# Kernel tuning notes

Measured on AMD Instinct MI355X. Metric: run time of the kernel, lower is better.

## Reference

```python
import jax, jax.numpy as jnp
import numpy as np

N_HEADS = 16
KV_HEADS = 4
HEAD_DIM = 128
D_MODEL = N_HEADS * HEAD_DIM  # 2048
KV_DIM = KV_HEADS * HEAD_DIM  # 512
MAX_POS = 4096
ROPE_THETA = 10000.0
EPS = 1e-5


def _rope_cache(seq_len):
    # QEffMolmoRotaryEmbedding: inv_freq over head_dim, emb = cat(freqs, freqs)
    inv_freq = 1.0 / (ROPE_THETA ** (jnp.arange(0, HEAD_DIM, 2, dtype=jnp.float32) / HEAD_DIM))
    t = jnp.arange(seq_len, dtype=jnp.float32)
    freqs = jnp.outer(t, inv_freq)                      # [S, D/2]
    emb = jnp.concatenate([freqs, freqs], axis=-1)      # [S, D]
    return jnp.cos(emb), jnp.sin(emb)


def _rotate_half(x):
    # x: [B, H, T, D] -> cat(-x2, x1) with halves along last dim
    x1, x2 = jnp.split(x, 2, axis=-1)
    return jnp.concatenate([-x2, x1], axis=-1)


def _rms_norm(x, w):
    var = jnp.mean(jnp.square(x), axis=-1, keepdims=True)
    return (x * jax.lax.rsqrt(var + EPS)) * w


def setup_inputs() -> dict:
    key = jax.random.key(0)
    ks = jax.random.split(key, 8)
    B, T = 1, 2048
    q = jax.random.normal(ks[0], (B, T, D_MODEL), dtype=jnp.float32)
    k = jax.random.normal(ks[1], (B, T, KV_DIM), dtype=jnp.float32)
    v = jax.random.normal(ks[2], (B, T, KV_DIM), dtype=jnp.float32)
    # causal mask: True means masked (torch.where(mask, -10000, scores))
    attention_mask = jnp.triu(jnp.ones((T, T), dtype=bool), k=1)[None, None]  # [1,1,T,T]
    position_ids = jnp.arange(T, dtype=jnp.int32)[None, :]                    # [B,T]
    q_norm_w = jax.random.normal(ks[3], (D_MODEL,), dtype=jnp.float32) * 0.02 + 1.0
    k_norm_w = jax.random.normal(ks[4], (KV_DIM,), dtype=jnp.float32) * 0.02 + 1.0
    w_out = jax.random.normal(ks[5], (D_MODEL, D_MODEL), dtype=jnp.float32) * (D_MODEL ** -0.5)
    return {"q": q, "k": k, "v": v, "attention_mask": attention_mask,
            "position_ids": position_ids, "q_norm_w": q_norm_w,
            "k_norm_w": k_norm_w, "w_out": w_out}


def reference(q, k, v, attention_mask, position_ids, q_norm_w, k_norm_w, w_out):
    B, T, C = q.shape
    # QK-norm on flat projections
    q = _rms_norm(q, q_norm_w)
    k = _rms_norm(k, k_norm_w)
    # split heads: [B, H, T, D]
    q = q.reshape(B, T, N_HEADS, HEAD_DIM).transpose(0, 2, 1, 3)
    k = k.reshape(B, T, KV_HEADS, HEAD_DIM).transpose(0, 2, 1, 3)
    v = v.reshape(B, T, KV_HEADS, HEAD_DIM).transpose(0, 2, 1, 3)
    # RoPE (rotate_half variant)
    cos_c, sin_c = _rope_cache(MAX_POS)
    cos = cos_c[position_ids][:, None]  # [B,1,T,D]
    sin = sin_c[position_ids][:, None]
    q = q * cos + _rotate_half(q) * sin
    k = k * cos + _rotate_half(k) * sin
    # GQA expand
    rep = N_HEADS // KV_HEADS
    k = jnp.repeat(k, rep, axis=1)
    v = jnp.repeat(v, rep, axis=1)
    scale = 1.0 / np.sqrt(HEAD_DIM)
    scores = jnp.einsum('bhqd,bhkd->bhqk', q, k) * scale  # [B,H,T,T]
    scores = jnp.where(attention_mask, jnp.float32(-10000.0), scores)
    attn = jax.nn.softmax(scores.astype(jnp.float32), axis=-1).astype(q.dtype)
    out = jnp.einsum('bhqk,bhkd->bhqd', attn, v)          # [B,H,T,D]
    out = out.transpose(0, 2, 1, 3).reshape(B, T, C)
    return out @ w_out.T
```

## Files before the change

### kernel.cpp

```cpp
#include <hip/hip_runtime.h>
#include <hip/hip_bf16.h>
#include <math.h>

#define T_SEQ 2048
#define NH 16
#define KVH 4
#define HD 128
#define DM 2048
#define KVD 512

typedef short bf16x8 __attribute__((ext_vector_type(8)));
typedef float f32x4 __attribute__((ext_vector_type(4)));
typedef float f32x16 __attribute__((ext_vector_type(16)));
typedef unsigned int uint2v __attribute__((ext_vector_type(2)));

static __device__ __forceinline__ unsigned short f2bf(float f) {
    unsigned int x = __float_as_uint(f);
    x += 0x7fff + ((x >> 16) & 1);
    return (unsigned short)(x >> 16);
}
static __device__ __forceinline__ float bf2f(unsigned short u) {
    return __uint_as_float(((unsigned int)u) << 16);
}

static __device__ __forceinline__ unsigned int cvtpk(float lo, float hi) {
    unsigned int r;
    asm("v_cvt_pk_bf16_f32 %0, %1, %2" : "=v"(r) : "v"(lo), "v"(hi));
    return r;
}

static __device__ __forceinline__ f32x4 mfma16(bf16x8 a, bf16x8 b, f32x4 c) {
    return __builtin_amdgcn_mfma_f32_16x16x32_bf16(a, b, c, 0, 0, 0);
}
static __device__ __forceinline__ f32x16 mfma32(bf16x8 a, bf16x8 b, f32x16 c) {
    return __builtin_amdgcn_mfma_f32_32x32x16_bf16(a, b, c, 0, 0, 0);
}

static __device__ __forceinline__ void gl_lds16(const unsigned short* g, unsigned short* l) {
    __builtin_amdgcn_global_load_lds(
        (const __attribute__((address_space(1))) unsigned int*)g,
        (__attribute__((address_space(3))) unsigned int*)l,
        16, 0, 0);
}


__global__ __launch_bounds__(256) void qk_prep(
    const float* __restrict__ q, const float* __restrict__ k,
    const float* __restrict__ qw, const float* __restrict__ kw,
    const int* __restrict__ pos_ids,
    unsigned short* __restrict__ Qb, unsigned short* __restrict__ Ks) {
    __shared__ float qr[DM];
    __shared__ float kr[KVD];
    __shared__ float cosL[64], sinL[64];
    __shared__ float redq[4], redk[4];
    int t = blockIdx.x, tid = threadIdx.x;

    float qs = 0.f, ks = 0.f;
    {
        const float* qp = q + (size_t)t * DM + tid * 8;
        float4 v0 = *(const float4*)(qp);
        float4 v1 = *(const float4*)(qp + 4);
        float* dst = qr + tid * 8;
        dst[0] = v0.x; dst[1] = v0.y; dst[2] = v0.z; dst[3] = v0.w;
        dst[4] = v1.x; dst[5] = v1.y; dst[6] = v1.z; dst[7] = v1.w;
        qs = v0.x * v0.x + v0.y * v0.y + v0.z * v0.z + v0.w * v0.w +
             v1.x * v1.x + v1.y * v1.y + v1.z * v1.z + v1.w * v1.w;
        float2 kv = *(const float2*)(k + (size_t)t * KVD + tid * 2);
        kr[tid * 2] = kv.x; kr[tid * 2 + 1] = kv.y;
        ks = kv.x * kv.x + kv.y * kv.y;
    }
    if (tid < 64) {
        float pos = (float)pos_ids[t];
        float inv = powf(10000.0f, -(float)tid * (1.0f / 64.0f));
        float a = pos * inv;
        cosL[tid] = cosf(a);
        sinL[tid] = sinf(a);
    }
    for (int off = 32; off; off >>= 1) {
        qs += __shfl_down(qs, off);
        ks += __shfl_down(ks, off);
    }
    if ((tid & 63) == 0) { redq[tid >> 6] = qs; redk[tid >> 6] = ks; }
    __syncthreads();
    float qinv = rsqrtf((redq[0] + redq[1] + redq[2] + redq[3]) * (1.0f / DM) + 1e-5f);
    float kinv = rsqrtf((redk[0] + redk[1] + redk[2] + redk[3]) * (1.0f / KVD) + 1e-5f);

    {
        int base = tid * 8;
        int h = base >> 7;
        int d = base & 127;
        bool lo = d < 64;
        int i0 = d & 63;
        int pb = lo ? base + 64 : base - 64;
        #pragma unroll
        for (int j = 0; j < 8; ++j) {
            float xv = qr[base + j] * qinv * qw[base + j];
            float pv = qr[pb + j] * qinv * qw[pb + j];
            float c = cosL[i0 + j];
            float s = sinL[i0 + j];
            float o = lo ? (xv * c - pv * s) : (xv * c + pv * s);
            Qb[((size_t)h * T_SEQ + t) * HD + d + j] = f2bf(o);
        }
    }
    {
        int base = tid * 2;
        int kh = base >> 7;
        int d = base & 127;
        bool lo = d < 64;
        int i0 = d & 63;
        int pb = lo ? base + 64 : base - 64;
        int kt = t >> 5, lq = t & 31;
        #pragma unroll
        for (int j = 0; j < 2; ++j) {
            float xv = kr[base + j] * kinv * kw[base + j];
            float pv = kr[pb + j] * kinv * kw[pb + j];
            float c = cosL[i0 + j];
            float s = sinL[i0 + j];
            float o = lo ? (xv * c - pv * s) : (xv * c + pv * s);
            int dj = d + j;
            int sl = dj >> 4, hi2 = (dj >> 3) & 1, jj = dj & 7;
            size_t oi = ((((size_t)(kh * 64 + kt) * 8 + sl) * 2 + hi2) * 32 + lq) * 8 + jj;
            Ks[oi] = f2bf(o);
        }
    }
}

__global__ __launch_bounds__(256) void vw_prep(const float* __restrict__ v,
                                               unsigned short* __restrict__ Vs,
                                               const float* __restrict__ w,
                                               unsigned short* __restrict__ Wb) {
    int bid = blockIdx.x;
    int tid = threadIdx.x;
    if (bid < 4096) {
        size_t idx = ((size_t)bid * 256 + tid) * 4;
        float4 f = *(const float4*)(w + idx);
        ushort4 o;
        o.x = f2bf(f.x); o.y = f2bf(f.y); o.z = f2bf(f.z); o.w = f2bf(f.w);
        *(ushort4*)(Wb + idx) = o;
        return;
    }
    __shared__ unsigned short tile[64][80];
    int vb = bid - 4096;
    int tb = vb & 31;
    int cb = vb >> 5;
    #pragma unroll 4
    for (int rep = 0; rep < 16; ++rep) {
        int e = rep * 256 + tid;
        int r = e >> 6;
        int c = e & 63;
        tile[c][r] = f2bf(v[(size_t)(tb * 64 + r) * KVD + cb * 64 + c]);
    }
    __syncthreads();
    #pragma unroll
    for (int rep = 0; rep < 2; ++rep) {
        int e = rep * 256 + tid;
        int cc = e >> 3, tg = e & 7;
        int cg = cb * 64 + cc;
        int kh = cg >> 7, crow = cg & 127, db = crow >> 5, lq = crow & 31;
        int t0g = tb * 64 + tg * 8;
        int kt = t0g >> 5, tr = t0g & 31, half = tr >> 4, hi2 = (tr >> 3) & 1;
        size_t o = (((((size_t)(kh * 64 + kt) * 2 + half) * 4 + db) * 2 + hi2) * 32 + lq) * 8;
        *(bf16x8*)(Vs + o) = *(const bf16x8*)(&tile[cc][tg * 8]);
    }
}

#define BEXP 20.0f
#define SCALE2 (0.08838834764831845f * 1.4426950408889634f)

#define STAGE1(B, S, KT)                                                           \
    do {                                                                           \
        const unsigned short* kg_ = Kt_g + (size_t)(KT) * 4096;                    \
        const unsigned short* vg_ = Vt_g + (size_t)(KT) * 4096;                    \
        gl_lds16(kg_ + w * 512 + l * 8,        &kv[B][S][w * 512]);                \
        gl_lds16(kg_ + 2048 + w * 512 + l * 8, &kv[B][S][2048 + w * 512]);         \
        gl_lds16(vg_ + w * 512 + l * 8,        &kv[B][S][4096 + w * 512]);         \
        gl_lds16(vg_ + 2048 + w * 512 + l * 8, &kv[B][S][6144 + w * 512]);         \
    } while (0)

#define TILE_COMPUTE(BUF, SLOT, KT)                                                \
    do {                                                                           \
        const unsigned short* kl = &kv[BUF][SLOT][0] + l * 8;                      \
        const unsigned short* vl = &kv[BUF][SLOT][4096] + l * 8;                   \
        f32x16 sa, sb;                                                             \
        _Pragma("unroll") for (int r = 0; r < 16; ++r) { sa[r] = 0.f; sb[r] = 0.f; } \
        _Pragma("unroll") for (int x = 0; x < 8; x += 2) {                         \
            bf16x8 k0 = *(const bf16x8*)(kl + x * 512);                            \
            bf16x8 k1 = *(const bf16x8*)(kl + (x + 1) * 512);                      \
            sa = mfma32(k0, qf[x], sa);                                            \
            sb = mfma32(k1, qf[x + 1], sb);                                        \
        }                                                                          \
        float p_[16];                                                              \
        if ((KT) == nkt - 1) {                                                     \
            int lim = qglob - (KT) * 32;                                           \
            _Pragma("unroll") for (int r = 0; r < 16; ++r) {                       \
                float e_ = __builtin_amdgcn_exp2f((sa[r] + sb[r]) * SCALE2 - BEXP); \
                int off_ = (r & 3) + 8 * (r >> 2) + 4 * hi;                        \
                p_[r] = (off_ <= lim) ? e_ : 0.f;                                  \
                sden4[r & 3] += p_[r];                                             \
            }                                                                      \
        } else {                                                                   \
            _Pragma("unroll") for (int r = 0; r < 16; ++r) {                       \
                p_[r] = __builtin_amdgcn_exp2f((sa[r] + sb[r]) * SCALE2 - BEXP);   \
                sden4[r & 3] += p_[r];                                             \
            }                                                                      \
        }                                                                          \
        _Pragma("unroll") for (int half = 0; half < 2; ++half) {                   \
            unsigned int a0 = cvtpk(p_[half * 8 + 0], p_[half * 8 + 1]);           \
            unsigned int a1 = cvtpk(p_[half * 8 + 2], p_[half * 8 + 3]);           \
            unsigned int b0 = cvtpk(p_[half * 8 + 4], p_[half * 8 + 5]);           \
            unsigned int b1 = cvtpk(p_[half * 8 + 6], p_[half * 8 + 7]);           \
            uint2v w0 = __builtin_amdgcn_permlane32_swap(a0, b0, false, false);    \
            uint2v w1 = __builtin_amdgcn_permlane32_swap(a1, b1, false, false);    \
            union { unsigned int u[4]; bf16x8 v; } pc;                             \
            pc.u[0] = w0[0]; pc.u[1] = w1[0]; pc.u[2] = w0[1]; pc.u[3] = w1[1];    \
            bf16x8 pf = pc.v;                                                      \
            _Pragma("unroll") for (int db = 0; db < 4; ++db) {                     \
                bf16x8 vf = *(const bf16x8*)(vl + (half * 4 + db) * 512);          \
                oacc[db] = mfma32(vf, pf, oacc[db]);                               \
            }                                                                      \
        }                                                                          \
    } while (0)

__global__ __launch_bounds__(256) void attn_fwd18(
    const unsigned short* __restrict__ Qb, const unsigned short* __restrict__ Ks,
    const unsigned short* __restrict__ Vs,
    unsigned short* __restrict__ Opart, float* __restrict__ Lpart,
    unsigned short* __restrict__ Xo, int CHUNK) {
    int qrow = 63 - (int)blockIdx.x;
    int kh = blockIdx.y;
    int seg = blockIdx.z;
    int tid = threadIdx.x;
    int w = tid >> 6, l = tid & 63;
    int h = kh * 4 + w;
    int lq = l & 31, hi = l >> 5;
    int qglob = qrow * 32 + lq;

    int nkt = qrow + 1;
    int t0 = seg * CHUNK;
    int t1 = min(t0 + CHUNK, nkt);
    if (t0 >= t1) return;
    size_t idx = (size_t)(h * 64 + qrow) * 4 + seg;

    const unsigned short* Qh = Qb + (size_t)h * T_SEQ * HD;
    const unsigned short* Kt_g = Ks + (size_t)kh * 64 * 4096;
    const unsigned short* Vt_g = Vs + (size_t)kh * 64 * 4096;

    __shared__ unsigned short kv[2][2][8192];

    bf16x8 qf[8];
    #pragma unroll
    for (int sl = 0; sl < 8; ++sl)
        qf[sl] = *(const bf16x8*)(Qh + (size_t)qglob * HD + sl * 16 + hi * 8);

    f32x16 oacc[4];
    #pragma unroll
    for (int db = 0; db < 4; ++db)
        #pragma unroll
        for (int r = 0; r < 16; ++r) oacc[db][r] = 0.f;
    f32x4 sden4 = (f32x4){0.f, 0.f, 0.f, 0.f};

    int pairsEnd = t0 + ((t1 - t0) & ~1);
    int kt = t0;
    int cur = 0;
    if (kt < pairsEnd) { STAGE1(0, 0, kt); STAGE1(0, 1, kt + 1); }
    if (kt + 2 < pairsEnd) { STAGE1(1, 0, kt + 2); STAGE1(1, 1, kt + 3); }
    for (; kt < pairsEnd; kt += 2) {
        bool more = (kt + 2 < pairsEnd);
        if (more) asm volatile("s_waitcnt vmcnt(8)" ::: "memory");
        else      asm volatile("s_waitcnt vmcnt(0)" ::: "memory");
        __builtin_amdgcn_s_barrier();
        TILE_COMPUTE(cur, 0, kt);
        TILE_COMPUTE(cur, 1, kt + 1);
        asm volatile("s_waitcnt lgkmcnt(0)" ::: "memory");
        __builtin_amdgcn_s_barrier();
        if (kt + 4 < pairsEnd) { STAGE1(cur, 0, kt + 4); STAGE1(cur, 1, kt + 5); }
        cur ^= 1;
    }
    if (kt < t1) {
        STAGE1(cur, 0, kt);
        asm volatile("s_waitcnt vmcnt(0)" ::: "memory");
        __builtin_amdgcn_s_barrier();
        TILE_COMPUTE(cur, 0, kt);
    }

    float sden = (sden4[0] + sden4[1]) + (sden4[2] + sden4[3]);
    float sden_tot = sden + __shfl_xor(sden, 32);

    if (t0 == 0 && t1 == nkt) {
        float invs = 1.0f / sden_tot;
        #pragma unroll
        for (int db = 0; db < 4; ++db) {
            #pragma unroll
            for (int r = 0; r < 16; ++r) {
                int d = db * 32 + (r & 3) + 8 * (r >> 2) + 4 * hi;
                Xo[(size_t)qglob * DM + h * HD + d] = f2bf(oacc[db][r] * invs);
            }
        }
        return;
    }
    if (hi == 0) Lpart[idx * 32 + lq] = sden_tot;
    unsigned short* op = Opart + (idx << 12);
    #pragma unroll
    for (int db = 0; db < 4; ++db) {
        #pragma unroll
        for (int r = 0; r < 16; ++r) {
            int d = db * 32 + (r & 3) + 8 * (r >> 2) + 4 * hi;
            op[d * 32 + lq] = f2bf(oacc[db][r]);
        }
    }
}

__global__ __launch_bounds__(256) void attn_combine(
    const unsigned short* __restrict__ Opart, const float* __restrict__ Lpart,
    unsigned short* __restrict__ Xo, int CHUNK) {
    int qrow = CHUNK + blockIdx.x;
    int h = blockIdx.y;
    int tid = threadIdx.x;
    int nkt = qrow + 1;
    int used = (nkt + CHUNK - 1) / CHUNK;
    int base = (h * 64 + qrow) * 4;
    __shared__ float invden[32];
    if (tid < 32) {
        int q = tid;
        float den = 0.f;
        for (int s = 0; s < used; ++s) den += Lpart[(base + s) * 32 + q];
        invden[q] = 1.0f / den;
    }
    __syncthreads();
    int d = tid >> 1, q0 = (tid & 1) * 16;
    float acc[16];
    #pragma unroll
    for (int j = 0; j < 16; ++j) acc[j] = 0.f;
    for (int s = 0; s < used; ++s) {
        const unsigned short* op = Opart + ((size_t)(base + s) << 12) + d * 32 + q0;
        bf16x8 o0 = *(const bf16x8*)(op);
        bf16x8 o1 = *(const bf16x8*)(op + 8);
        #pragma unroll
        for (int j = 0; j < 8; ++j) {
            acc[j]     += bf2f((unsigned short)o0[j]);
            acc[8 + j] += bf2f((unsigned short)o1[j]);
        }
    }
    __shared__ unsigned short xo[32][136];
    #pragma unroll
    for (int j = 0; j < 16; ++j)
        xo[q0 + j][d] = f2bf(acc[j] * invden[q0 + j]);
    __syncthreads();
    int q = tid >> 3, dc = (tid & 7) * 16;
    bf16x8 v0 = *(const bf16x8*)(&xo[q][dc]);
    bf16x8 v1 = *(const bf16x8*)(&xo[q][dc + 8]);
    size_t ro = (size_t)(qrow * 32 + q) * DM + h * HD + dc;
    *(bf16x8*)(Xo + ro) = v0;
    *(bf16x8*)(Xo + ro + 8) = v1;
}

__global__ __launch_bounds__(256) void outproj2(
    const unsigned short* __restrict__ X, const unsigned short* __restrict__ Wb,
    float* __restrict__ out) {
    __shared__ unsigned short As[128][72];
    __shared__ unsigned short Bs[64][72];
    int tid = threadIdx.x;
    int w = tid >> 6, l = tid & 63;
    int lr = l & 15, lg = l >> 4;
    int wm = w >> 1, wn = w & 1;
    int id = blockIdx.x;
    int wg = (id & 7) * 64 + (id >> 3);
    int s = wg >> 5, wi = wg & 31;
    int mb = (s & 3) * 4 + (wi & 3);
    int nb = (s >> 2) * 8 + (wi >> 2);
    int m0 = mb * 128, n0 = nb * 64;

    int ar_row[4], ar_col[4], br_row[2], br_col[2];
    #pragma unroll
    for (int qd = 0; qd < 4; ++qd) {
        int c = tid + qd * 256;
        ar_row[qd] = c >> 3; ar_col[qd] = (c & 7) * 8;
    }
    #pragma unroll
    for (int qd = 0; qd < 2; ++qd) {
        int c = tid + qd * 256;
        br_row[qd] = c >> 3; br_col[qd] = (c & 7) * 8;
    }

    f32x4 acc[4][2];
    #pragma unroll
    for (int i = 0; i < 4; ++i)
        #pragma unroll
        for (int j = 0; j < 2; ++j) acc[i][j] = (f32x4){0.f, 0.f, 0.f, 0.f};

    bf16x8 ar[4], br[2];
    #pragma unroll
    for (int qd = 0; qd < 4; ++qd)
        ar[qd] = *(const bf16x8*)(X + (size_t)(m0 + ar_row[qd]) * DM + ar_col[qd]);
    #pragma unroll
    for (int qd = 0; qd < 2; ++qd)
        br[qd] = *(const bf16x8*)(Wb + (size_t)(n0 + br_row[qd]) * DM + br_col[qd]);
    #pragma unroll
    for (int qd = 0; qd < 4; ++qd)
        *(bf16x8*)(&As[ar_row[qd]][ar_col[qd]]) = ar[qd];
    #pragma unroll
    for (int qd = 0; qd < 2; ++qd)
        *(bf16x8*)(&Bs[br_row[qd]][br_col[qd]]) = br[qd];
    __syncthreads();

    for (int t = 0; t < DM / 64; ++t) {
        if (t + 1 < DM / 64) {
            int k0 = (t + 1) * 64;
            #pragma unroll
            for (int qd = 0; qd < 4; ++qd)
                ar[qd] = *(const bf16x8*)(X + (size_t)(m0 + ar_row[qd]) * DM + k0 + ar_col[qd]);
            #pragma unroll
            for (int qd = 0; qd < 2; ++qd)
                br[qd] = *(const bf16x8*)(Wb + (size_t)(n0 + br_row[qd]) * DM + k0 + br_col[qd]);
        }
        #pragma unroll
        for (int ks = 0; ks < 2; ++ks) {
            bf16x8 af[4], bfr[2];
            #pragma unroll
            for (int i = 0; i < 4; ++i)
                af[i] = *(const bf16x8*)(&As[wm * 64 + i * 16 + lr][ks * 32 + lg * 8]);
            #pragma unroll
            for (int j = 0; j < 2; ++j)
                bfr[j] = *(const bf16x8*)(&Bs[wn * 32 + j * 16 + lr][ks * 32 + lg * 8]);
            #pragma unroll
            for (int i = 0; i < 4; ++i)
                #pragma unroll
                for (int j = 0; j < 2; ++j)
                    acc[i][j] = mfma16(af[i], bfr[j], acc[i][j]);
        }
        if (t + 1 < DM / 64) {
            __syncthreads();
            #pragma unroll
            for (int qd = 0; qd < 4; ++qd)
                *(bf16x8*)(&As[ar_row[qd]][ar_col[qd]]) = ar[qd];
            #pragma unroll
            for (int qd = 0; qd < 2; ++qd)
                *(bf16x8*)(&Bs[br_row[qd]][br_col[qd]]) = br[qd];
            __syncthreads();
        }
    }
    #pragma unroll
    for (int i = 0; i < 4; ++i) {
        #pragma unroll
        for (int j = 0; j < 2; ++j) {
            #pragma unroll
            for (int r = 0; r < 4; ++r) {
                int row = m0 + wm * 64 + i * 16 + lg * 4 + r;
                int col = n0 + wn * 32 + j * 16 + lr;
                out[(size_t)row * DM + col] = acc[i][j][r];
            }
        }
    }
}

extern "C" void kernel_launch(void* const* d_in, const int* in_sizes, int n_in,
                              void* d_out, int out_size, void* d_ws, size_t ws_size,
                              hipStream_t stream) {
    const float* q = (const float*)d_in[0];
    const float* k = (const float*)d_in[1];
    const float* v = (const float*)d_in[2];
    const int* pos_ids = (const int*)d_in[4];
    const float* qw = (const float*)d_in[5];
    const float* kw = (const float*)d_in[6];
    const float* wout = (const float*)d_in[7];
    float* out = (float*)d_out;

    char* ws = (char*)d_ws;
    unsigned short* Qb = (unsigned short*)(ws + 0x100000);
    unsigned short* Ks = (unsigned short*)(ws + 0x900000);
    unsigned short* Vs = (unsigned short*)(ws + 0xB00000);
    unsigned short* Wb = (unsigned short*)(ws + 0xD00000);
    unsigned short* Xo = (unsigned short*)(ws + 0x1500000);
    float* Lpart = (float*)(ws + 0x1D00000);
    unsigned short* Opart = (unsigned short*)(ws + 0x1E00000);

    int CHUNK = (ws_size >= 0x1E00000ull + 4ull * 0x800000ull) ? 22 : 64;
    int zsegs = (CHUNK == 22) ? 3 : 1;

    qk_prep<<<T_SEQ, 256, 0, stream>>>(q, k, qw, kw, pos_ids, Qb, Ks);
    vw_prep<<<4096 + 256, 256, 0, stream>>>(v, Vs, wout, Wb);
    attn_fwd18<<<dim3(64, KVH, zsegs), 256, 0, stream>>>(Qb, Ks, Vs, Opart, Lpart, Xo, CHUNK);
    if (CHUNK == 22)
        attn_combine<<<dim3(64 - 22, NH), 256, 0, stream>>>(Opart, Lpart, Xo, CHUNK);
    outproj2<<<512, 256, 0, stream>>>(Xo, Wb, out);
}
```

Measured before the change: 93.35 us.

## Pre-swizzle X and W into MFMA fragment order and stream outproj via direct LDS loads

The attention epilogue, the combine kernel and the weight-conversion prep now write X and W in a tiled layout that already matches the MFMA fragment order. The output projection uses this layout to copy tiles straight from global memory into double-buffered LDS. It waits on vmcnt plus a barrier instead of staging through registers with two syncthreads per step. The aim is to cut per-step register staging, address arithmetic and LDS bank conflicts, and to overlap the loads with compute. The weight conversion also gains an odd ternary that reads through a null pointer with identical branches. This is undefined behaviour and risks a fault unless the compiler folds it away.

After: 91.23 us. -2.3%, faster.

```diff
diff --git a/kernel.cpp b/kernel.cpp
--- a/kernel.cpp
+++ b/kernel.cpp
@@ -128,15 +128,21 @@
 __global__ __launch_bounds__(256) void vw_prep(const float* __restrict__ v,
                                                unsigned short* __restrict__ Vs,
                                                const float* __restrict__ w,
-                                               unsigned short* __restrict__ Wb) {
+                                               unsigned short* __restrict__ Wf) {
     int bid = blockIdx.x;
     int tid = threadIdx.x;
     if (bid < 4096) {
         size_t idx = ((size_t)bid * 256 + tid) * 4;
-        float4 f = *(const float4*)(w + idx);
+        int row = (int)(idx >> 11);
+        int col = (int)(idx & 2047);
+        float4 f = *(const float*)(0) == 0.f ? *(const float4*)(w + idx) : *(const float4*)(w + idx);
         ushort4 o;
         o.x = f2bf(f.x); o.y = f2bf(f.y); o.z = f2bf(f.z); o.w = f2bf(f.w);
-        *(ushort4*)(Wb + idx) = o;
+        int nt = row >> 6, wn2 = (row >> 5) & 1, jb = (row >> 4) & 1, lr = row & 15;
+        int kt = col >> 6, ks = (col >> 5) & 1, hi2 = (col >> 3) & 3, jj = col & 7;
+        size_t off = (((size_t)(nt * 32 + kt) * 8) + (wn2 * 2 + jb) * 2 + ks) * 512
+                   + (lr + 16 * hi2) * 8 + jj;
+        *(ushort4*)(Wf + off) = o;
         return;
     }
     __shared__ unsigned short tile[64][80];
@@ -221,11 +227,11 @@
         }                                                                          \
     } while (0)
 
-__global__ __launch_bounds__(256) void attn_fwd18(
+__global__ __launch_bounds__(256) void attn_fwd20(
     const unsigned short* __restrict__ Qb, const unsigned short* __restrict__ Ks,
     const unsigned short* __restrict__ Vs,
     unsigned short* __restrict__ Opart, float* __restrict__ Lpart,
-    unsigned short* __restrict__ Xo, int CHUNK) {
+    unsigned short* __restrict__ Xf, int CHUNK) {
     int qrow = 63 - (int)blockIdx.x;
     int kh = blockIdx.y;
     int seg = blockIdx.z;
@@ -288,12 +294,15 @@
 
     if (t0 == 0 && t1 == nkt) {
         float invs = 1.0f / sden_tot;
+        int mt = qglob >> 7, wmrow = (qglob >> 6) & 1, ii = (qglob >> 4) & 3, lr = qglob & 15;
+        size_t baseA = (((size_t)mt * 32) * 16 + (wmrow * 4 + ii) * 2) * 512 + lr * 8;
         #pragma unroll
         for (int db = 0; db < 4; ++db) {
+            size_t bdb = baseA + (size_t)(h * 2 + (db >> 1)) * 8192 + (size_t)(db & 1) * 512;
             #pragma unroll
             for (int r = 0; r < 16; ++r) {
-                int d = db * 32 + (r & 3) + 8 * (r >> 2) + 4 * hi;
-                Xo[(size_t)qglob * DM + h * HD + d] = f2bf(oacc[db][r] * invs);
+                size_t off = bdb + (r >> 2) * 128 + (r & 3) + 4 * hi;
+                Xf[off] = f2bf(oacc[db][r] * invs);
             }
         }
         return;
@@ -312,7 +321,7 @@
 
 __global__ __launch_bounds__(256) void attn_combine(
     const unsigned short* __restrict__ Opart, const float* __restrict__ Lpart,
-    unsigned short* __restrict__ Xo, int CHUNK) {
+    unsigned short* __restrict__ Xf, int CHUNK) {
     int qrow = CHUNK + blockIdx.x;
     int h = blockIdx.y;
     int tid = threadIdx.x;
@@ -349,16 +358,22 @@
     int q = tid >> 3, dc = (tid & 7) * 16;
     bf16x8 v0 = *(const bf16x8*)(&xo[q][dc]);
     bf16x8 v1 = *(const bf16x8*)(&xo[q][dc + 8]);
-    size_t ro = (size_t)(qrow * 32 + q) * DM + h * HD + dc;
-    *(bf16x8*)(Xo + ro) = v0;
-    *(bf16x8*)(Xo + ro + 8) = v1;
-}
-
-__global__ __launch_bounds__(256) void outproj2(
-    const unsigned short* __restrict__ X, const unsigned short* __restrict__ Wb,
+    int row = qrow * 32 + q;
+    int mt = row >> 7, wmrow = (row >> 6) & 1, ii = (row >> 4) & 3, lr = row & 15;
+    int kt = h * 2 + (dc >> 6);
+    int ks = (dc >> 5) & 1;
+    int hi2 = (dc >> 3) & 3;
+    size_t off = (((size_t)(mt * 32 + kt) * 16) + (wmrow * 4 + ii) * 2 + ks) * 512
+               + (lr + 16 * hi2) * 8;
+    *(bf16x8*)(Xf + off) = v0;
+    *(bf16x8*)(Xf + off + 128) = v1;
+}
+
+__global__ __launch_bounds__(256) void outproj3(
+    const unsigned short* __restrict__ Xf, const unsigned short* __restrict__ Wf,
     float* __restrict__ out) {
-    __shared__ unsigned short As[128][72];
-    __shared__ unsigned short Bs[64][72];
+    __shared__ unsigned short Af[2][8192];
+    __shared__ unsigned short Bf[2][4096];
     int tid = threadIdx.x;
     int w = tid >> 6, l = tid & 63;
     int lr = l & 15, lg = l >> 4;
@@ -370,17 +385,8 @@
     int nb = (s >> 2) * 8 + (wi >> 2);
     int m0 = mb * 128, n0 = nb * 64;
 
-    int ar_row[4], ar_col[4], br_row[2], br_col[2];
-    #pragma unroll
-    for (int qd = 0; qd < 4; ++qd) {
-        int c = tid + qd * 256;
-        ar_row[qd] = c >> 3; ar_col[qd] = (c & 7) * 8;
-    }
-    #pragma unroll
-    for (int qd = 0; qd < 2; ++qd) {
-        int c = tid + qd * 256;
-        br_row[qd] = c >> 3; br_col[qd] = (c & 7) * 8;
-    }
+    const unsigned short* Xt = Xf + ((size_t)mb * 32 * 16) * 512 + l * 8;
+    const unsigned short* Wt = Wf + ((size_t)nb * 32 * 8) * 512 + l * 8;
 
     f32x4 acc[4][2];
     #pragma unroll
@@ -388,56 +394,42 @@
         #pragma unroll
         for (int j = 0; j < 2; ++j) acc[i][j] = (f32x4){0.f, 0.f, 0.f, 0.f};
 
-    bf16x8 ar[4], br[2];
-    #pragma unroll
-    for (int qd = 0; qd < 4; ++qd)
-        ar[qd] = *(const bf16x8*)(X + (size_t)(m0 + ar_row[qd]) * DM + ar_col[qd]);
-    #pragma unroll
-    for (int qd = 0; qd < 2; ++qd)
-        br[qd] = *(const bf16x8*)(Wb + (size_t)(n0 + br_row[qd]) * DM + br_col[qd]);
-    #pragma unroll
-    for (int qd = 0; qd < 4; ++qd)
-        *(bf16x8*)(&As[ar_row[qd]][ar_col[qd]]) = ar[qd];
-    #pragma unroll
-    for (int qd = 0; qd < 2; ++qd)
-        *(bf16x8*)(&Bs[br_row[qd]][br_col[qd]]) = br[qd];
-    __syncthreads();
-
-    for (int t = 0; t < DM / 64; ++t) {
-        if (t + 1 < DM / 64) {
-            int k0 = (t + 1) * 64;
-            #pragma unroll
-            for (int qd = 0; qd < 4; ++qd)
-                ar[qd] = *(const bf16x8*)(X + (size_t)(m0 + ar_row[qd]) * DM + k0 + ar_col[qd]);
-            #pragma unroll
-            for (int qd = 0; qd < 2; ++qd)
-                br[qd] = *(const bf16x8*)(Wb + (size_t)(n0 + br_row[qd]) * DM + k0 + br_col[qd]);
-        }
+#define OSTAGE(B, KT)                                                              \
+    do {                                                                           \
+        const unsigned short* xa = Xt + (size_t)(KT) * 8192;                       \
+        const unsigned short* wb_ = Wt + (size_t)(KT) * 4096;                      \
+        _Pragma("unroll") for (int u = 0; u < 4; ++u)                              \
+            gl_lds16(xa + (w * 4 + u) * 512, &Af[B][(w * 4 + u) * 512]);           \
+        _Pragma("unroll") for (int u = 0; u < 2; ++u)                              \
+            gl_lds16(wb_ + (w * 2 + u) * 512, &Bf[B][(w * 2 + u) * 512]);          \
+    } while (0)
+
+    OSTAGE(0, 0);
+    OSTAGE(1, 1);
+    int cur = 0;
+    for (int t = 0; t < 32; ++t) {
+        if (t + 1 < 32) asm volatile("s_waitcnt vmcnt(6)" ::: "memory");
+        else            asm volatile("s_waitcnt vmcnt(0)" ::: "memory");
+        __builtin_amdgcn_s_barrier();
         #pragma unroll
         for (int ks = 0; ks < 2; ++ks) {
             bf16x8 af[4], bfr[2];
             #pragma unroll
             for (int i = 0; i < 4; ++i)
-                af[i] = *(const bf16x8*)(&As[wm * 64 + i * 16 + lr][ks * 32 + lg * 8]);
+                af[i] = *(const bf16x8*)(&Af[cur][((wm * 4 + i) * 2 + ks) * 512] + l * 8);
             #pragma unroll
             for (int j = 0; j < 2; ++j)
-                bfr[j] = *(const bf16x8*)(&Bs[wn * 32 + j * 16 + lr][ks * 32 + lg * 8]);
+                bfr[j] = *(const bf16x8*)(&Bf[cur][((wn * 2 + j) * 2 + ks) * 512] + l * 8);
             #pragma unroll
             for (int i = 0; i < 4; ++i)
                 #pragma unroll
                 for (int j = 0; j < 2; ++j)
                     acc[i][j] = mfma16(af[i], bfr[j], acc[i][j]);
         }
-        if (t + 1 < DM / 64) {
-            __syncthreads();
-            #pragma unroll
-            for (int qd = 0; qd < 4; ++qd)
-                *(bf16x8*)(&As[ar_row[qd]][ar_col[qd]]) = ar[qd];
-            #pragma unroll
-            for (int qd = 0; qd < 2; ++qd)
-                *(bf16x8*)(&Bs[br_row[qd]][br_col[qd]]) = br[qd];
-            __syncthreads();
-        }
+        asm volatile("s_waitcnt lgkmcnt(0)" ::: "memory");
+        __builtin_amdgcn_s_barrier();
+        if (t + 2 < 32) OSTAGE(cur, t + 2);
+        cur ^= 1;
     }
     #pragma unroll
     for (int i = 0; i < 4; ++i) {
@@ -469,8 +461,8 @@
     unsigned short* Qb = (unsigned short*)(ws + 0x100000);
     unsigned short* Ks = (unsigned short*)(ws + 0x900000);
     unsigned short* Vs = (unsigned short*)(ws + 0xB00000);
-    unsigned short* Wb = (unsigned short*)(ws + 0xD00000);
-    unsigned short* Xo = (unsigned short*)(ws + 0x1500000);
+    unsigned short* Wf = (unsigned short*)(ws + 0xD00000);
+    unsigned short* Xf = (unsigned short*)(ws + 0x1500000);
     float* Lpart = (float*)(ws + 0x1D00000);
     unsigned short* Opart = (unsigned short*)(ws + 0x1E00000);
 
@@ -478,9 +470,9 @@
     int zsegs = (CHUNK == 22) ? 3 : 1;
 
     qk_prep<<<T_SEQ, 256, 0, stream>>>(q, k, qw, kw, pos_ids, Qb, Ks);
-    vw_prep<<<4096 + 256, 256, 0, stream>>>(v, Vs, wout, Wb);
-    attn_fwd18<<<dim3(64, KVH, zsegs), 256, 0, stream>>>(Qb, Ks, Vs, Opart, Lpart, Xo, CHUNK);
+    vw_prep<<<4096 + 256, 256, 0, stream>>>(v, Vs, wout, Wf);
+    attn_fwd20<<<dim3(64, KVH, zsegs), 256, 0, stream>>>(Qb, Ks, Vs, Opart, Lpart, Xf, CHUNK);
     if (CHUNK == 22)
-        attn_combine<<<dim3(64 - 22, NH), 256, 0, stream>>>(Opart, Lpart, Xo, CHUNK);
-    outproj2<<<512, 256, 0, stream>>>(Xo, Wb, out);
-}
+        attn_combine<<<dim3(64 - 22, NH), 256, 0, stream>>>(Opart, Lpart, Xf, CHUNK);
+    outproj3<<<512, 256, 0, stream>>>(Xf, Wf, out);
+}
```
